# Performance work log

Measured on AMD Instinct MI355X. Metric: run time of the kernel, lower is better.

Reference implementation:

```python
import jax, jax.numpy as jnp
import numpy as np

EMBED_DIM = 512
NUM_JOINTS = 17
HIDDEN = EMBED_DIM * 2  # hidden_ratio=2
B, T = 32, 243


def setup_inputs() -> dict:
    key = jax.random.key(0)
    k_x, k_w1, k_w2 = jax.random.split(key, 3)
    x = jax.random.normal(k_x, (B, T, NUM_JOINTS, EMBED_DIM), dtype=jnp.float32)
    # kaiming_uniform with a=sqrt(5): bound = sqrt(6 / ((1 + a^2) * fan_in)) = sqrt(1/fan_in)
    b1 = float(np.sqrt(1.0 / EMBED_DIM))
    fc1_w = jax.random.uniform(k_w1, (NUM_JOINTS, EMBED_DIM, HIDDEN), minval=-b1, maxval=b1, dtype=jnp.float32)
    fc1_b = jnp.zeros((NUM_JOINTS, HIDDEN), dtype=jnp.float32)
    b2 = float(np.sqrt(1.0 / HIDDEN))
    fc2_w = jax.random.uniform(k_w2, (NUM_JOINTS, HIDDEN, 3), minval=-b2, maxval=b2, dtype=jnp.float32)
    fc2_b = jnp.zeros((NUM_JOINTS, 3), dtype=jnp.float32)
    ln_gamma = jnp.ones((EMBED_DIM,), dtype=jnp.float32)
    ln_beta = jnp.zeros((EMBED_DIM,), dtype=jnp.float32)
    return {"x": x, "ln_gamma": ln_gamma, "ln_beta": ln_beta,
            "fc1_w": fc1_w, "fc1_b": fc1_b, "fc2_w": fc2_w, "fc2_b": fc2_b}


def _layernorm(x, gamma, beta, eps=1e-5):
    mu = jnp.mean(x, axis=-1, keepdims=True)
    var = jnp.mean(jnp.square(x - mu), axis=-1, keepdims=True)
    return (x - mu) * jax.lax.rsqrt(var + eps) * gamma + beta


def reference(x, ln_gamma, ln_beta, fc1_w, fc1_b, fc2_w, fc2_b):
    # x: [B, T, J, d] -> [B, T, J, 3]
    xn = _layernorm(x, ln_gamma, ln_beta)
    h = jnp.einsum('btjd,jdh->btjh', xn, fc1_w) + fc1_b  # [B,T,J,H]
    h = jax.nn.gelu(h, approximate=False)  # torch GELU default is exact (erf)
    y = jnp.einsum('btjh,jho->btjo', h, fc2_w) + fc2_b  # [B,T,J,3]
    return y
```

## Files before the change

kernel.cpp:

```cpp
#include <hip/hip_runtime.h>
#include <hip/hip_bf16.h>

#define JN   17
#define DIM  512
#define HID  1024
#define MTOT 7776
#define BM   128
#define BN   256
#define BK   32
#define NTHR 512

typedef __attribute__((ext_vector_type(8))) short s16x8;
typedef __attribute__((ext_vector_type(4))) float f32x4;
typedef unsigned short ushort_t;

__device__ __forceinline__ unsigned int f2bf(float f) {
    return (unsigned int)__builtin_bit_cast(unsigned short, __float2bfloat16(f));
}

__device__ __forceinline__ float gelu_erf(float h) {
    float ah = fabsf(h);
    float z  = ah * 0.7071067811865476f;
    float t  = __builtin_amdgcn_rcpf(fmaf(0.3275911f, z, 1.0f));
    float p  = fmaf(fmaf(fmaf(fmaf(1.061405429f, t, -1.453152027f), t,
                              1.421413741f), t, -0.284496736f), t, 0.254829592f);
    float er = 1.0f - p * t * __expf(-z * z);
    return fmaf(0.5f * ah, er, 0.5f * h);
}

__global__ __launch_bounds__(256)
void prep_w1(const float* __restrict__ w1, ushort_t* __restrict__ w1s) {
    int b  = blockIdx.x;
    int nq = b & 3;
    int kc = (b >> 2) & 15;
    int j  = b >> 6;
    int n  = nq * 256 + threadIdx.x;

    const float* src = w1 + ((size_t)j * DIM + kc * 32) * HID + n;
    ushort_t* dst = w1s + (((size_t)j * 16 + kc) * 1024 + n) * 32;

    #pragma unroll
    for (int u = 0; u < 4; ++u) {
        float v[8];
        #pragma unroll
        for (int e = 0; e < 8; ++e) v[e] = src[(u * 8 + e) * HID];
        uint4 qq;
        qq.x = f2bf(v[0]) | (f2bf(v[1]) << 16);
        qq.y = f2bf(v[2]) | (f2bf(v[3]) << 16);
        qq.z = f2bf(v[4]) | (f2bf(v[5]) << 16);
        qq.w = f2bf(v[6]) | (f2bf(v[7]) << 16);
        int p = u ^ ((n >> 1) & 3);
        *(uint4*)(dst + p * 8) = qq;
    }
}

#define A_OFF 0
#define B_OFF 131072
#define Y_OFF 131072
#define SMEM_V2 163840

__global__ __launch_bounds__(NTHR, 2)
void pjh_fused_v2(const float* __restrict__ x,
                  const float* __restrict__ gamma,
                  const float* __restrict__ beta,
                  const ushort_t* __restrict__ w1s,
                  const float* __restrict__ b1,
                  const float* __restrict__ w2,
                  const float* __restrict__ b2,
                  float* __restrict__ out)
{
    extern __shared__ char smem[];
    const int tid  = threadIdx.x;
    const int lane = tid & 63;
    const int wv   = tid >> 6;
    const int wm   = wv >> 2;
    const int wn   = wv & 3;
    const int mt   = blockIdx.x;
    const int j    = blockIdx.y;

    const ushort_t* w1j = w1s + (size_t)j * 16 * 1024 * 32;

    {
        const ushort_t* tb = w1j;
        #pragma unroll
        for (int q = 0; q < 2; ++q) {
            const ushort_t* src = tb + (size_t)(wv * 2 + q) * 512 + lane * 8;
            void* dst = smem + B_OFF + (wv * 2 + q) * 1024;
            __builtin_amdgcn_global_load_lds(
                (const __attribute__((address_space(1))) unsigned int*)src,
                (__attribute__((address_space(3))) unsigned int*)dst, 16, 0, 0);
        }
    }

    {
        const float4* gp  = (const float4*)(gamma + lane * 8);
        const float4* bpp = (const float4*)(beta + lane * 8);
        float4 g0 = gp[0], g1 = gp[1];
        float4 e0 = bpp[0], e1 = bpp[1];
        #pragma unroll 1
        for (int rb = 0; rb < 16; rb += 4) {
            float4 xs[4][2];
            #pragma unroll
            for (int r = 0; r < 4; ++r) {
                int gr = mt * BM + wv * 16 + rb + r;
                if (gr < MTOT) {
                    const float4* xp = (const float4*)(x + ((size_t)gr * JN + j) * DIM + lane * 8);
                    xs[r][0] = xp[0]; xs[r][1] = xp[1];
                } else {
                    xs[r][0] = make_float4(0.f,0.f,0.f,0.f);
                    xs[r][1] = make_float4(0.f,0.f,0.f,0.f);
                }
            }
            #pragma unroll
            for (int r = 0; r < 4; ++r) {
                int m = wv * 16 + rb + r;
                float4 xa = xs[r][0], xb = xs[r][1];
                float s  = ((xa.x + xa.y) + (xa.z + xa.w)) + ((xb.x + xb.y) + (xb.z + xb.w));
                float s2 = fmaf(xa.x, xa.x, fmaf(xa.y, xa.y, fmaf(xa.z, xa.z, fmaf(xa.w, xa.w,
                           fmaf(xb.x, xb.x, fmaf(xb.y, xb.y, fmaf(xb.z, xb.z, xb.w * xb.w)))))));
                #pragma unroll
                for (int d = 1; d < 64; d <<= 1) {
                    s  += __shfl_xor(s,  d);
                    s2 += __shfl_xor(s2, d);
                }
                float mu  = s * (1.0f / 512.0f);
                float var = s2 * (1.0f / 512.0f) - mu * mu;
                float rs  = rsqrtf(var + 1e-5f);
                float v0 = fmaf((xa.x - mu) * rs, g0.x, e0.x);
                float v1 = fmaf((xa.y - mu) * rs, g0.y, e0.y);
                float v2 = fmaf((xa.z - mu) * rs, g0.z, e0.z);
                float v3 = fmaf((xa.w - mu) * rs, g0.w, e0.w);
                float v4 = fmaf((xb.x - mu) * rs, g1.x, e1.x);
                float v5 = fmaf((xb.y - mu) * rs, g1.y, e1.y);
                float v6 = fmaf((xb.z - mu) * rs, g1.z, e1.z);
                float v7 = fmaf((xb.w - mu) * rs, g1.w, e1.w);
                uint4 qq;
                qq.x = f2bf(v0) | (f2bf(v1) << 16);
                qq.y = f2bf(v2) | (f2bf(v3) << 16);
                qq.z = f2bf(v4) | (f2bf(v5) << 16);
                qq.w = f2bf(v6) | (f2bf(v7) << 16);
                *(uint4*)(smem + A_OFF + m * 1024 + ((lane ^ (m & 7)) * 16)) = qq;
            }
        }
    }

    __syncthreads();

    float yr[4][4][3];
    #pragma unroll
    for (int a = 0; a < 4; ++a)
        #pragma unroll
        for (int r = 0; r < 4; ++r)
            #pragma unroll
            for (int o = 0; o < 3; ++o) yr[a][r][o] = 0.f;

    const f32x4 zero4 = {0.f, 0.f, 0.f, 0.f};
    f32x4 acc[4][4];
    #pragma unroll
    for (int mf = 0; mf < 4; ++mf)
        #pragma unroll
        for (int nf = 0; nf < 4; ++nf) acc[mf][nf] = zero4;

    #pragma unroll 1
    for (int t = 0; t < 64; ++t) {
        if (t + 1 < 64) {
            int kc = (t + 1) & 15, nt = (t + 1) >> 4;
            const ushort_t* tb = w1j + ((size_t)kc * 1024 + nt * 256) * 32;
            int bb = ((t + 1) & 1) * 16384;
            #pragma unroll
            for (int q = 0; q < 2; ++q) {
                const ushort_t* src = tb + (size_t)(wv * 2 + q) * 512 + lane * 8;
                void* dst = smem + B_OFF + bb + (wv * 2 + q) * 1024;
                __builtin_amdgcn_global_load_lds(
                    (const __attribute__((address_space(1))) unsigned int*)src,
                    (__attribute__((address_space(3))) unsigned int*)dst, 16, 0, 0);
            }
        }

        int kc = t & 15;
        int bb = (t & 1) * 16384;
        int g  = lane >> 4;
        s16x8 aF[4], bF[4];
        #pragma unroll
        for (int mf = 0; mf < 4; ++mf) {
            int m  = wm * 64 + mf * 16 + (lane & 15);
            int ul = kc * 4 + g;
            aF[mf] = *(const s16x8*)(smem + A_OFF + m * 1024 + ((ul ^ (m & 7)) * 16));
        }
        #pragma unroll
        for (int nf = 0; nf < 4; ++nf) {
            int nl = wn * 64 + nf * 16 + (lane & 15);
            int p  = g ^ ((nl >> 1) & 3);
            bF[nf] = *(const s16x8*)(smem + B_OFF + bb + (nl * 4 + p) * 16);
        }
        #pragma unroll
        for (int mf = 0; mf < 4; ++mf)
            #pragma unroll
            for (int nf = 0; nf < 4; ++nf)
                acc[mf][nf] = __builtin_amdgcn_mfma_f32_16x16x32_bf16(aF[mf], bF[nf], acc[mf][nf], 0, 0, 0);

        if ((t & 15) == 15) {
            int nt = t >> 4;
            #pragma unroll
            for (int nf = 0; nf < 4; ++nf) {
                int n = nt * BN + wn * 64 + nf * 16 + (lane & 15);
                float b1v = b1[j * HID + n];
                const float* w2p = w2 + ((size_t)j * HID + n) * 3;
                float w20 = w2p[0], w21 = w2p[1], w22 = w2p[2];
                #pragma unroll
                for (int mf = 0; mf < 4; ++mf) {
                    #pragma unroll
                    for (int r = 0; r < 4; ++r) {
                        float gv = gelu_erf(acc[mf][nf][r] + b1v);
                        yr[mf][r][0] = fmaf(gv, w20, yr[mf][r][0]);
                        yr[mf][r][1] = fmaf(gv, w21, yr[mf][r][1]);
                        yr[mf][r][2] = fmaf(gv, w22, yr[mf][r][2]);
                    }
                }
            }
            #pragma unroll
            for (int mf = 0; mf < 4; ++mf)
                #pragma unroll
                for (int nf = 0; nf < 4; ++nf)
                    acc[mf][nf] = zero4;
        }
        __syncthreads();
    }

    #pragma unroll
    for (int mf = 0; mf < 4; ++mf)
        #pragma unroll
        for (int r = 0; r < 4; ++r)
            #pragma unroll
            for (int o = 0; o < 3; ++o) {
                float v = yr[mf][r][o];
                v += __shfl_xor(v, 1);
                v += __shfl_xor(v, 2);
                v += __shfl_xor(v, 4);
                v += __shfl_xor(v, 8);
                yr[mf][r][o] = v;
            }

    float* Yp = (float*)(smem + Y_OFF);
    if ((lane & 15) == 0) {
        int mrow = lane >> 4;
        #pragma unroll
        for (int mf = 0; mf < 4; ++mf)
            #pragma unroll
            for (int r = 0; r < 4; ++r) {
                int m = wm * 64 + mf * 16 + mrow * 4 + r;
                #pragma unroll
                for (int o = 0; o < 3; ++o)
                    Yp[(wn * BM + m) * 3 + o] = yr[mf][r][o];
            }
    }
    __syncthreads();

    if (tid < BM * 3) {
        int m = tid / 3;
        int o = tid - m * 3;
        int gr = mt * BM + m;
        if (gr < MTOT) {
            float v = Yp[m * 3 + o] + Yp[(BM + m) * 3 + o]
                    + Yp[(2 * BM + m) * 3 + o] + Yp[(3 * BM + m) * 3 + o]
                    + b2[j * 3 + o];
            out[((size_t)gr * JN + j) * 3 + o] = v;
        }
    }
}

#define A1_OFF 0
#define B1_OFF 131072
#define Y1_OFF 147456
#define SMEM_V1 153600

__global__ __launch_bounds__(NTHR, 2)
void pjh_fused_v1(const float* __restrict__ x,
                  const float* __restrict__ gamma,
                  const float* __restrict__ beta,
                  const float* __restrict__ w1,
                  const float* __restrict__ b1,
                  const float* __restrict__ w2,
                  const float* __restrict__ b2,
                  float* __restrict__ out)
{
    extern __shared__ char smem[];
    const int tid  = threadIdx.x;
    const int lane = tid & 63;
    const int wv   = tid >> 6;
    const int wm   = wv >> 2;
    const int wn   = wv & 3;
    const int mt   = blockIdx.x;
    const int j    = blockIdx.y;
    const int t2 = tid >> 7;
    const int n2 = (tid & 127) * 2;
    const float* w1j = w1 + (size_t)j * DIM * HID;

    float la[8][2];
    {
        const float* bp = w1j + (size_t)(8 * t2) * HID + n2;
        #pragma unroll
        for (int i = 0; i < 8; ++i) { la[i][0] = bp[i * HID + 0]; la[i][1] = bp[i * HID + 1]; }
    }
    {
        const float4* gp = (const float4*)(gamma + lane * 8);
        const float4* bpp = (const float4*)(beta + lane * 8);
        float4 g0 = gp[0], g1 = gp[1];
        float4 e0 = bpp[0], e1 = bpp[1];
        #pragma unroll 1
        for (int rr = 0; rr < 16; ++rr) {
            int m  = wv * 16 + rr;
            int gr = mt * BM + m;
            float4 xa = {0.f,0.f,0.f,0.f}, xb = {0.f,0.f,0.f,0.f};
            if (gr < MTOT) {
                const float4* xp = (const float4*)(x + ((size_t)gr * JN + j) * DIM + lane * 8);
                xa = xp[0]; xb = xp[1];
            }
            float s  = ((xa.x + xa.y) + (xa.z + xa.w)) + ((xb.x + xb.y) + (xb.z + xb.w));
            float s2 = fmaf(xa.x, xa.x, fmaf(xa.y, xa.y, fmaf(xa.z, xa.z, fmaf(xa.w, xa.w,
                       fmaf(xb.x, xb.x, fmaf(xb.y, xb.y, fmaf(xb.z, xb.z, xb.w * xb.w)))))));
            #pragma unroll
            for (int d = 1; d < 64; d <<= 1) { s += __shfl_xor(s, d); s2 += __shfl_xor(s2, d); }
            float mu  = s * (1.0f / 512.0f);
            float var = s2 * (1.0f / 512.0f) - mu * mu;
            float rs  = rsqrtf(var + 1e-5f);
            uint4 qq = {0u,0u,0u,0u};
            if (gr < MTOT) {
                float v0 = fmaf((xa.x - mu) * rs, g0.x, e0.x);
                float v1 = fmaf((xa.y - mu) * rs, g0.y, e0.y);
                float v2 = fmaf((xa.z - mu) * rs, g0.z, e0.z);
                float v3 = fmaf((xa.w - mu) * rs, g0.w, e0.w);
                float v4 = fmaf((xb.x - mu) * rs, g1.x, e1.x);
                float v5 = fmaf((xb.y - mu) * rs, g1.y, e1.y);
                float v6 = fmaf((xb.z - mu) * rs, g1.z, e1.z);
                float v7 = fmaf((xb.w - mu) * rs, g1.w, e1.w);
                qq.x = f2bf(v0) | (f2bf(v1) << 16);
                qq.y = f2bf(v2) | (f2bf(v3) << 16);
                qq.z = f2bf(v4) | (f2bf(v5) << 16);
                qq.w = f2bf(v6) | (f2bf(v7) << 16);
            }
            *(uint4*)(smem + A1_OFF + m * 1024 + ((lane ^ (m & 7)) * 16)) = qq;
        }
    }

    float yr[4][4][3];
    #pragma unroll
    for (int a = 0; a < 4; ++a)
        #pragma unroll
        for (int r = 0; r < 4; ++r)
            #pragma unroll
            for (int o = 0; o < 3; ++o) yr[a][r][o] = 0.f;
    const f32x4 zero4 = {0.f,0.f,0.f,0.f};

    #pragma unroll 1
    for (int nt = 0; nt < 4; ++nt) {
        f32x4 acc[4][4];
        #pragma unroll
        for (int mf = 0; mf < 4; ++mf)
            #pragma unroll
            for (int nf = 0; nf < 4; ++nf) acc[mf][nf] = zero4;
        #pragma unroll 1
        for (int kci = 0; kci < 16; ++kci) {
            __syncthreads();
            #pragma unroll
            for (int u = 0; u < 2; ++u) {
                int n = n2 + u;
                uint4 qq;
                qq.x = f2bf(la[0][u]) | (f2bf(la[1][u]) << 16);
                qq.y = f2bf(la[2][u]) | (f2bf(la[3][u]) << 16);
                qq.z = f2bf(la[4][u]) | (f2bf(la[5][u]) << 16);
                qq.w = f2bf(la[6][u]) | (f2bf(la[7][u]) << 16);
                int phys = t2 ^ ((n >> 1) & 3);
                *(uint4*)(smem + B1_OFF + n * 64 + phys * 16) = qq;
            }
            __syncthreads();
            int gt = nt * 16 + kci;
            if (gt + 1 < 64) {
                int nnt = (gt + 1) >> 4;
                int nkc = ((gt + 1) & 15) * BK;
                const float* bp = w1j + (size_t)(nkc + 8 * t2) * HID + nnt * BN + n2;
                #pragma unroll
                for (int i = 0; i < 8; ++i) { la[i][0] = bp[i * HID + 0]; la[i][1] = bp[i * HID + 1]; }
            }
            int kc = kci * BK;
            s16x8 aF[4], bF[4];
            #pragma unroll
            for (int mf = 0; mf < 4; ++mf) {
                int m  = wm * 64 + mf * 16 + (lane & 15);
                int ul = (kc >> 3) + (lane >> 4);
                aF[mf] = *(const s16x8*)(smem + A1_OFF + m * 1024 + ((ul ^ (m & 7)) * 16));
            }
            #pragma unroll
            for (int nf = 0; nf < 4; ++nf) {
                int n  = wn * 64 + nf * 16 + (lane & 15);
                int ph = (lane >> 4) ^ ((n >> 1) & 3);
                bF[nf] = *(const s16x8*)(smem + B1_OFF + n * 64 + ph * 16);
            }
            #pragma unroll
            for (int mf = 0; mf < 4; ++mf)
                #pragma unroll
                for (int nf = 0; nf < 4; ++nf)
                    acc[mf][nf] = __builtin_amdgcn_mfma_f32_16x16x32_bf16(aF[mf], bF[nf], acc[mf][nf], 0, 0, 0);
        }
        #pragma unroll
        for (int nf = 0; nf < 4; ++nf) {
            int n = nt * BN + wn * 64 + nf * 16 + (lane & 15);
            float b1v = b1[j * HID + n];
            const float* w2p = w2 + ((size_t)j * HID + n) * 3;
            float w20 = w2p[0], w21 = w2p[1], w22 = w2p[2];
            #pragma unroll
            for (int mf = 0; mf < 4; ++mf)
                #pragma unroll
                for (int r = 0; r < 4; ++r) {
                    float gv = gelu_erf(acc[mf][nf][r] + b1v);
                    yr[mf][r][0] = fmaf(gv, w20, yr[mf][r][0]);
                    yr[mf][r][1] = fmaf(gv, w21, yr[mf][r][1]);
                    yr[mf][r][2] = fmaf(gv, w22, yr[mf][r][2]);
                }
        }
    }
    #pragma unroll
    for (int mf = 0; mf < 4; ++mf)
        #pragma unroll
        for (int r = 0; r < 4; ++r)
            #pragma unroll
            for (int o = 0; o < 3; ++o) {
                float v = yr[mf][r][o];
                v += __shfl_xor(v, 1); v += __shfl_xor(v, 2);
                v += __shfl_xor(v, 4); v += __shfl_xor(v, 8);
                yr[mf][r][o] = v;
            }
    float* Yp = (float*)(smem + Y1_OFF);
    if ((lane & 15) == 0) {
        int mrow = lane >> 4;
        #pragma unroll
        for (int mf = 0; mf < 4; ++mf)
            #pragma unroll
            for (int r = 0; r < 4; ++r) {
                int m = wm * 64 + mf * 16 + mrow * 4 + r;
                #pragma unroll
                for (int o = 0; o < 3; ++o) Yp[(wn * BM + m) * 3 + o] = yr[mf][r][o];
            }
    }
    __syncthreads();
    if (tid < BM * 3) {
        int m = tid / 3;
        int o = tid - m * 3;
        int gr = mt * BM + m;
        if (gr < MTOT) {
            float v = Yp[m * 3 + o] + Yp[(BM + m) * 3 + o]
                    + Yp[(2 * BM + m) * 3 + o] + Yp[(3 * BM + m) * 3 + o]
                    + b2[j * 3 + o];
            out[((size_t)gr * JN + j) * 3 + o] = v;
        }
    }
}

extern "C" void kernel_launch(void* const* d_in, const int* in_sizes, int n_in,
                              void* d_out, int out_size, void* d_ws, size_t ws_size,
                              hipStream_t stream) {
    (void)in_sizes; (void)n_in; (void)out_size;
    const float* x   = (const float*)d_in[0];
    const float* ga  = (const float*)d_in[1];
    const float* be  = (const float*)d_in[2];
    const float* w1  = (const float*)d_in[3];
    const float* b1  = (const float*)d_in[4];
    const float* w2  = (const float*)d_in[5];
    const float* b2  = (const float*)d_in[6];
    float* out = (float*)d_out;

    const size_t w1s_bytes = (size_t)JN * 16 * 1024 * 4 * 8 * sizeof(ushort_t);

    if (ws_size >= w1s_bytes) {
        ushort_t* w1s = (ushort_t*)d_ws;
        prep_w1<<<JN * 16 * 4, 256, 0, stream>>>(w1, w1s);
        hipFuncSetAttribute((const void*)pjh_fused_v2,
                            hipFuncAttributeMaxDynamicSharedMemorySize, SMEM_V2);
        dim3 grid((MTOT + BM - 1) / BM, JN);
        pjh_fused_v2<<<grid, NTHR, SMEM_V2, stream>>>(x, ga, be, w1s, b1, w2, b2, out);
    } else {
        hipFuncSetAttribute((const void*)pjh_fused_v1,
                            hipFuncAttributeMaxDynamicSharedMemorySize, SMEM_V1);
        dim3 grid((MTOT + BM - 1) / BM, JN);
        pjh_fused_v1<<<grid, NTHR, SMEM_V1, stream>>>(x, ga, be, w1, b1, w2, b2, out);
    }
}
```

Before: 344.6 us.

## Shrink M tile to 96 rows and deepen W1 prefetch to quad-buffered ring

Changes the row tile from 128 to 96. Since 96 divides 7776 exactly, the grid needs no partial tiles and the bounds checks are dropped. The freed LDS holds a 4-slot W1 ring prefetched two steps ahead, and the full __syncthreads is replaced with a partial vmcnt wait plus a raw barrier so loads overlap the MFMA work. It also raises wave priority around the MFMA block. The smaller tile gives more blocks (81x17), which helps balance across CUs, but lowers MFMA reuse of each B fragment per block.

```diff
diff --git a/kernel.cpp b/kernel.cpp
--- a/kernel.cpp
+++ b/kernel.cpp
@@ -5,7 +5,6 @@
 #define DIM  512
 #define HID  1024
 #define MTOT 7776
-#define BM   128
 #define BN   256
 #define BK   32
 #define NTHR 512
@@ -54,13 +53,14 @@
     }
 }
 
-#define A_OFF 0
-#define B_OFF 131072
-#define Y_OFF 131072
-#define SMEM_V2 163840
+#define BM3 96
+#define A3_OFF 0
+#define B3_OFF 98304
+#define Y3_OFF 98304
+#define SMEM_V3 163840
 
 __global__ __launch_bounds__(NTHR, 2)
-void pjh_fused_v2(const float* __restrict__ x,
+void pjh_fused_v3(const float* __restrict__ x,
                   const float* __restrict__ gamma,
                   const float* __restrict__ beta,
                   const ushort_t* __restrict__ w1s,
@@ -80,12 +80,14 @@
 
     const ushort_t* w1j = w1s + (size_t)j * 16 * 1024 * 32;
 
-    {
-        const ushort_t* tb = w1j;
+    #pragma unroll
+    for (int tt = 0; tt < 2; ++tt) {
+        int kc = tt & 15, nt = 0;
+        const ushort_t* tb = w1j + ((size_t)kc * 1024 + nt * 256) * 32;
         #pragma unroll
         for (int q = 0; q < 2; ++q) {
             const ushort_t* src = tb + (size_t)(wv * 2 + q) * 512 + lane * 8;
-            void* dst = smem + B_OFF + (wv * 2 + q) * 1024;
+            void* dst = smem + B3_OFF + tt * 16384 + (wv * 2 + q) * 1024;
             __builtin_amdgcn_global_load_lds(
                 (const __attribute__((address_space(1))) unsigned int*)src,
                 (__attribute__((address_space(3))) unsigned int*)dst, 16, 0, 0);
@@ -97,23 +99,18 @@
         const float4* bpp = (const float4*)(beta + lane * 8);
         float4 g0 = gp[0], g1 = gp[1];
         float4 e0 = bpp[0], e1 = bpp[1];
-        #pragma unroll 1
-        for (int rb = 0; rb < 16; rb += 4) {
+        #pragma unroll
+        for (int rb = 0; rb < 12; rb += 4) {
             float4 xs[4][2];
             #pragma unroll
             for (int r = 0; r < 4; ++r) {
-                int gr = mt * BM + wv * 16 + rb + r;
-                if (gr < MTOT) {
-                    const float4* xp = (const float4*)(x + ((size_t)gr * JN + j) * DIM + lane * 8);
-                    xs[r][0] = xp[0]; xs[r][1] = xp[1];
-                } else {
-                    xs[r][0] = make_float4(0.f,0.f,0.f,0.f);
-                    xs[r][1] = make_float4(0.f,0.f,0.f,0.f);
-                }
+                int gr = mt * BM3 + wv * 12 + rb + r;
+                const float4* xp = (const float4*)(x + ((size_t)gr * JN + j) * DIM + lane * 8);
+                xs[r][0] = xp[0]; xs[r][1] = xp[1];
             }
             #pragma unroll
             for (int r = 0; r < 4; ++r) {
-                int m = wv * 16 + rb + r;
+                int m = wv * 12 + rb + r;
                 float4 xa = xs[r][0], xb = xs[r][1];
                 float s  = ((xa.x + xa.y) + (xa.z + xa.w)) + ((xb.x + xb.y) + (xb.z + xb.w));
                 float s2 = fmaf(xa.x, xa.x, fmaf(xa.y, xa.y, fmaf(xa.z, xa.z, fmaf(xa.w, xa.w,
@@ -139,38 +136,38 @@
                 qq.y = f2bf(v2) | (f2bf(v3) << 16);
                 qq.z = f2bf(v4) | (f2bf(v5) << 16);
                 qq.w = f2bf(v6) | (f2bf(v7) << 16);
-                *(uint4*)(smem + A_OFF + m * 1024 + ((lane ^ (m & 7)) * 16)) = qq;
+                *(uint4*)(smem + A3_OFF + m * 1024 + ((lane ^ (m & 7)) * 16)) = qq;
             }
         }
     }
 
     __syncthreads();
 
-    float yr[4][4][3];
-    #pragma unroll
-    for (int a = 0; a < 4; ++a)
+    float yr[3][4][3];
+    #pragma unroll
+    for (int a = 0; a < 3; ++a)
         #pragma unroll
         for (int r = 0; r < 4; ++r)
             #pragma unroll
             for (int o = 0; o < 3; ++o) yr[a][r][o] = 0.f;
 
     const f32x4 zero4 = {0.f, 0.f, 0.f, 0.f};
-    f32x4 acc[4][4];
-    #pragma unroll
-    for (int mf = 0; mf < 4; ++mf)
+    f32x4 acc[3][4];
+    #pragma unroll
+    for (int mf = 0; mf < 3; ++mf)
         #pragma unroll
         for (int nf = 0; nf < 4; ++nf) acc[mf][nf] = zero4;
 
     #pragma unroll 1
     for (int t = 0; t < 64; ++t) {
-        if (t + 1 < 64) {
-            int kc = (t + 1) & 15, nt = (t + 1) >> 4;
+        if (t + 2 < 64) {
+            int kc = (t + 2) & 15, nt = (t + 2) >> 4;
             const ushort_t* tb = w1j + ((size_t)kc * 1024 + nt * 256) * 32;
-            int bb = ((t + 1) & 1) * 16384;
+            int bb = ((t + 2) & 3) * 16384;
             #pragma unroll
             for (int q = 0; q < 2; ++q) {
                 const ushort_t* src = tb + (size_t)(wv * 2 + q) * 512 + lane * 8;
-                void* dst = smem + B_OFF + bb + (wv * 2 + q) * 1024;
+                void* dst = smem + B3_OFF + bb + (wv * 2 + q) * 1024;
                 __builtin_amdgcn_global_load_lds(
                     (const __attribute__((address_space(1))) unsigned int*)src,
                     (__attribute__((address_space(3))) unsigned int*)dst, 16, 0, 0);
@@ -178,26 +175,29 @@
         }
 
         int kc = t & 15;
-        int bb = (t & 1) * 16384;
+        int bb = (t & 3) * 16384;
         int g  = lane >> 4;
-        s16x8 aF[4], bF[4];
-        #pragma unroll
-        for (int mf = 0; mf < 4; ++mf) {
-            int m  = wm * 64 + mf * 16 + (lane & 15);
+        s16x8 aF[3], bF[4];
+        #pragma unroll
+        for (int mf = 0; mf < 3; ++mf) {
+            int m  = wm * 48 + mf * 16 + (lane & 15);
             int ul = kc * 4 + g;
-            aF[mf] = *(const s16x8*)(smem + A_OFF + m * 1024 + ((ul ^ (m & 7)) * 16));
+            aF[mf] = *(const s16x8*)(smem + A3_OFF + m * 1024 + ((ul ^ (m & 7)) * 16));
         }
         #pragma unroll
         for (int nf = 0; nf < 4; ++nf) {
             int nl = wn * 64 + nf * 16 + (lane & 15);
             int p  = g ^ ((nl >> 1) & 3);
-            bF[nf] = *(const s16x8*)(smem + B_OFF + bb + (nl * 4 + p) * 16);
-        }
-        #pragma unroll
-        for (int mf = 0; mf < 4; ++mf)
+            bF[nf] = *(const s16x8*)(smem + B3_OFF + bb + (nl * 4 + p) * 16);
+        }
+
+        __builtin_amdgcn_s_setprio(1);
+        #pragma unroll
+        for (int mf = 0; mf < 3; ++mf)
             #pragma unroll
             for (int nf = 0; nf < 4; ++nf)
                 acc[mf][nf] = __builtin_amdgcn_mfma_f32_16x16x32_bf16(aF[mf], bF[nf], acc[mf][nf], 0, 0, 0);
+        __builtin_amdgcn_s_setprio(0);
 
         if ((t & 15) == 15) {
             int nt = t >> 4;
@@ -208,7 +208,7 @@
                 const float* w2p = w2 + ((size_t)j * HID + n) * 3;
                 float w20 = w2p[0], w21 = w2p[1], w22 = w2p[2];
                 #pragma unroll
-                for (int mf = 0; mf < 4; ++mf) {
+                for (int mf = 0; mf < 3; ++mf) {
                     #pragma unroll
                     for (int r = 0; r < 4; ++r) {
                         float gv = gelu_erf(acc[mf][nf][r] + b1v);
@@ -219,16 +219,22 @@
                 }
             }
             #pragma unroll
-            for (int mf = 0; mf < 4; ++mf)
+            for (int mf = 0; mf < 3; ++mf)
                 #pragma unroll
                 for (int nf = 0; nf < 4; ++nf)
                     acc[mf][nf] = zero4;
         }
-        __syncthreads();
-    }
-
-    #pragma unroll
-    for (int mf = 0; mf < 4; ++mf)
+
+        if (t < 62) {
+            asm volatile("s_waitcnt vmcnt(2)" ::: "memory");
+        } else {
+            asm volatile("s_waitcnt vmcnt(0)" ::: "memory");
+        }
+        __builtin_amdgcn_s_barrier();
+    }
+
+    #pragma unroll
+    for (int mf = 0; mf < 3; ++mf)
         #pragma unroll
         for (int r = 0; r < 4; ++r)
             #pragma unroll
@@ -241,34 +247,35 @@
                 yr[mf][r][o] = v;
             }
 
-    float* Yp = (float*)(smem + Y_OFF);
+    __syncthreads();
+
+    float* Yp = (float*)(smem + Y3_OFF);
     if ((lane & 15) == 0) {
         int mrow = lane >> 4;
         #pragma unroll
-        for (int mf = 0; mf < 4; ++mf)
+        for (int mf = 0; mf < 3; ++mf)
             #pragma unroll
             for (int r = 0; r < 4; ++r) {
-                int m = wm * 64 + mf * 16 + mrow * 4 + r;
+                int m = wm * 48 + mf * 16 + mrow * 4 + r;
                 #pragma unroll
                 for (int o = 0; o < 3; ++o)
-                    Yp[(wn * BM + m) * 3 + o] = yr[mf][r][o];
+                    Yp[(wn * BM3 + m) * 3 + o] = yr[mf][r][o];
             }
     }
     __syncthreads();
 
-    if (tid < BM * 3) {
+    if (tid < BM3 * 3) {
         int m = tid / 3;
         int o = tid - m * 3;
-        int gr = mt * BM + m;
-        if (gr < MTOT) {
-            float v = Yp[m * 3 + o] + Yp[(BM + m) * 3 + o]
-                    + Yp[(2 * BM + m) * 3 + o] + Yp[(3 * BM + m) * 3 + o]
-                    + b2[j * 3 + o];
-            out[((size_t)gr * JN + j) * 3 + o] = v;
-        }
-    }
-}
-
+        int gr = mt * BM3 + m;
+        float v = Yp[m * 3 + o] + Yp[(BM3 + m) * 3 + o]
+                + Yp[(2 * BM3 + m) * 3 + o] + Yp[(3 * BM3 + m) * 3 + o]
+                + b2[j * 3 + o];
+        out[((size_t)gr * JN + j) * 3 + o] = v;
+    }
+}
+
+#define BM   128
 #define A1_OFF 0
 #define B1_OFF 131072
 #define Y1_OFF 147456
@@ -474,10 +481,10 @@
     if (ws_size >= w1s_bytes) {
         ushort_t* w1s = (ushort_t*)d_ws;
         prep_w1<<<JN * 16 * 4, 256, 0, stream>>>(w1, w1s);
-        hipFuncSetAttribute((const void*)pjh_fused_v2,
-                            hipFuncAttributeMaxDynamicSharedMemorySize, SMEM_V2);
-        dim3 grid((MTOT + BM - 1) / BM, JN);
-        pjh_fused_v2<<<grid, NTHR, SMEM_V2, stream>>>(x, ga, be, w1s, b1, w2, b2, out);
+        hipFuncSetAttribute((const void*)pjh_fused_v3,
+                            hipFuncAttributeMaxDynamicSharedMemorySize, SMEM_V3);
+        dim3 grid(MTOT / BM3, JN);
+        pjh_fused_v3<<<grid, NTHR, SMEM_V3, stream>>>(x, ga, be, w1s, b1, w2, b2, out);
     } else {
         hipFuncSetAttribute((const void*)pjh_fused_v1,
                             hipFuncAttributeMaxDynamicSharedMemorySize, SMEM_V1);
```

Measured after the change: 328.6 us. 4.7% less time.
